# Kernel optimization log

Measured on AMD Instinct MI355X. Metric: run time of the kernel, lower is better.

## Reference

```python
import jax, jax.numpy as jnp
import numpy as np
from jax.scipy.special import gammaln, digamma


def setup_inputs() -> dict:
    key = jax.random.key(0)
    k1, k2 = jax.random.split(key)
    N, M, D = 512, 512, 256
    # Dirichlet concentration parameters: strictly positive
    v_alpha = jax.random.uniform(k1, (N, D), dtype=jnp.float32)
    t_alpha = jax.random.uniform(k2, (M, D), dtype=jnp.float32)
    return {"v_alpha": v_alpha, "t_alpha": t_alpha}


def _compute_kl(v_alpha, t_alpha):
    # v_alpha, t_alpha broadcast to (..., D); returns (...,) KL(Dir(v)||Dir(t))
    eps = 1e-08
    v = v_alpha + eps
    t = t_alpha + eps
    sum_v = v.sum(axis=-1)
    sum_t = t.sum(axis=-1)
    first = (gammaln(t).sum(axis=-1) + gammaln(sum_v)
             - gammaln(sum_t) - gammaln(v).sum(axis=-1))
    second = ((v - t) * (digamma(v) - digamma(sum_v)[..., None])).sum(axis=-1)
    return first + second


def reference(v_alpha, t_alpha):
    # Pairwise JS divergence between all (t_row, v_row) pairs.
    # Original: v.repeat(M,1) / t.repeat_interleave(N) then view(M, N)
    # -> equivalent to broadcasting t over axis 0, v over axis 1.
    v = v_alpha[None, :, :]   # (1, N, D)
    t = t_alpha[:, None, :]   # (M, 1, D)
    m = 0.5 * (v + t)         # (M, N, D)
    jsd = 0.5 * _compute_kl(v, m) + 0.5 * _compute_kl(t, m)  # (M, N)
    return 1.0 - jsd
```

## Files before the change

### kernel.cpp

```cpp
#include <hip/hip_runtime.h>

#define D 256
#define NV 512
#define NT 512
#define KCAT 1536
#define EPS 1e-8f
#define HALF_EPS 5e-9f
#define LN2 0.69314718055994531f

#define C0 0.28468287047291920f
#define C1 0.70315664064524320f
#define C2 0.24517887805011740f
#define C3 (-0.03936734194028790f)
#define C4 0.00932941036738560f
#define C5 (-0.00261463332905590f)
#define C6 0.00080356830356760f
#define C0E 0.28460998445f
#define C1E 0.69577526404f
#define C2E 0.24751123064f

#define LSTRIDE 68

typedef float f32x4 __attribute__((ext_vector_type(4)));
typedef short s16x8 __attribute__((ext_vector_type(8)));
typedef unsigned short u16;

__device__ __forceinline__ float rcpf(float x) { return __builtin_amdgcn_rcpf(x); }

__device__ __forceinline__ u16 f2bf(float f) {
    unsigned int u = __float_as_uint(f);
    return (u16)((u + 0x7FFFu + ((u >> 16) & 1u)) >> 16);
}
__device__ __forceinline__ float bf2f(u16 b) {
    return __uint_as_float(((unsigned int)b) << 16);
}

__device__ __forceinline__ float stirling_lgamma(float y) {
    float r = rcpf(y), r2 = r * r;
    float ln = LN2 * __log2f(y);
    return (y - 0.5f) * ln - y + 0.91893853320467f
         + r * (0.08333333333f - 0.00277777778f * r2);
}

__device__ __forceinline__ float stirling_digamma(float y) {
    float r = rcpf(y), r2 = r * r;
    return LN2 * __log2f(y) - 0.5f * r - r2 * (0.08333333333f - 0.00833333333f * r2);
}

__global__ __launch_bounds__(256) void row_stats(
    const float* __restrict__ va, const float* __restrict__ ta,
    u16* __restrict__ Acat, u16* __restrict__ Bcat,
    float* __restrict__ rv, float* __restrict__ rt)
{
    int r = blockIdx.x;
    bool isV = (r < NV);
    int rr = isV ? r : r - NV;
    const float* row = (isV ? va : ta) + rr * D;
    float* sc = (isV ? rv : rt) + rr * 4;
    u16* cat = (isV ? Bcat : Acat) + rr * KCAT;

    int d = threadIdx.x;
    float raw = row[d];
    float x = raw + EPS;

    float y = x + 4.0f;
    float ry = rcpf(y), ry2 = ry * ry;
    float psi = LN2 * __log2f(y) - 0.5f * ry - ry2 * (0.08333333333f - 0.00833333333f * ry2);
    psi -= rcpf(x) + rcpf(x + 1.0f) + rcpf(x + 2.0f) + rcpf(x + 3.0f);

    float s = x - 0.5f;
    float q6 = fmaf(C6, s, C5);
    q6 = fmaf(q6, s, C4); q6 = fmaf(q6, s, C3); q6 = fmaf(q6, s, C2); q6 = fmaf(q6, s, C1);
    float g = fmaf(q6, s, C0) - LN2 * __log2f(x * (x + 1.0f));

    float pm = psi - C2E * x;
    u16 xh = f2bf(x);  u16 xl = f2bf(x - bf2f(xh));
    u16 ph = f2bf(pm); u16 pl = f2bf(pm - bf2f(ph));
    if (isV) {
        cat[d] = ph; cat[d+256] = pl; cat[d+512] = ph;
        cat[d+768] = xh; cat[d+1024] = xl; cat[d+1280] = xh;
    } else {
        cat[d] = xh; cat[d+256] = xh; cat[d+512] = xl;
        cat[d+768] = ph; cat[d+1024] = ph; cat[d+1280] = pl;
    }

    float vh = fmaf(0.5f, raw, HALF_EPS);
    float S = raw, G = g, P = x * psi, Q = vh * vh;
    #pragma unroll
    for (int off = 32; off > 0; off >>= 1) {
        S += __shfl_down(S, off, 64);
        G += __shfl_down(G, off, 64);
        P += __shfl_down(P, off, 64);
        Q += __shfl_down(Q, off, 64);
    }
    __shared__ float red[4][4];
    int wid = d >> 6, lane = d & 63;
    if (lane == 0) { red[0][wid] = S; red[1][wid] = G; red[2][wid] = P; red[3][wid] = Q; }
    __syncthreads();
    if (d == 0) {
        float S4 = red[0][0] + red[0][1] + red[0][2] + red[0][3];
        float G4 = red[1][0] + red[1][1] + red[1][2] + red[1][3];
        float P4 = red[2][0] + red[2][1] + red[2][2] + red[2][3];
        float Q4 = red[3][0] + red[3][1] + red[3][2] + red[3][3];
        float Se = S4 + 256.0f * EPS;
        float A = 0.5f * (stirling_lgamma(Se) - G4) + 0.25f * P4;
        *(float4*)sc = make_float4(S4, A, stirling_digamma(Se), Q4);
    }
}

__global__ __launch_bounds__(256, 4) void jsd_pairs(
    const float* __restrict__ va, const float* __restrict__ ta,
    const u16* __restrict__ Acat, const u16* __restrict__ Bcat,
    const float* __restrict__ rv, const float* __restrict__ rt,
    float* __restrict__ out)
{
    __shared__ float vs[16 * LSTRIDE];
    __shared__ float ts[16 * LSTRIDE];
    __shared__ float red[4 * 256];

    const int tid = threadIdx.x;
    const int j0 = blockIdx.x * 16;
    const int i0 = blockIdx.y * 16;
    const int w = tid >> 6, l = tid & 63;

    {
        f32x4 acc = {0.0f, 0.0f, 0.0f, 0.0f};
        const u16* Ap = Acat + (i0 + (l & 15)) * KCAT + w * 384 + ((l >> 4) << 3);
        const u16* Bp = Bcat + (j0 + (l & 15)) * KCAT + w * 384 + ((l >> 4) << 3);
        #pragma unroll
        for (int st = 0; st < 12; ++st) {
            s16x8 a = *(const s16x8*)(Ap + (st << 5));
            s16x8 b = *(const s16x8*)(Bp + (st << 5));
            acc = __builtin_amdgcn_mfma_f32_16x16x32_bf16(a, b, acc, 0, 0, 0);
        }
        int base = w * 256 + ((l >> 4) << 6) + (l & 15);
        red[base]      = acc[0];
        red[base + 16] = acc[1];
        red[base + 32] = acc[2];
        red[base + 48] = acc[3];
    }

    const int tj = tid & 15;
    const int ti = tid >> 4;
    const float* vp = vs + tj * LSTRIDE;
    const float* tp = ts + ti * LSTRIDE;
    const int ldst = ti * LSTRIDE + (tj << 2);

    float accLa = 0.0f, accLb = 0.0f;

    for (int h = 0; h < 4; ++h) {
        if (h) __syncthreads();
        {
            int goff = (h << 6) + (tj << 2);
            float4 a = *(const float4*)(va + (j0 + ti) * D + goff);
            float4 e = *(const float4*)(ta + (i0 + ti) * D + goff);
            a.x = fmaf(0.5f, a.x, HALF_EPS); a.y = fmaf(0.5f, a.y, HALF_EPS);
            a.z = fmaf(0.5f, a.z, HALF_EPS); a.w = fmaf(0.5f, a.w, HALF_EPS);
            e.x = fmaf(0.5f, e.x, HALF_EPS); e.y = fmaf(0.5f, e.y, HALF_EPS);
            e.z = fmaf(0.5f, e.z, HALF_EPS); e.w = fmaf(0.5f, e.w, HALF_EPS);
            *(float4*)(vs + ldst) = a;
            *(float4*)(ts + ldst) = e;
        }
        __syncthreads();

        #pragma unroll
        for (int c = 0; c < 16; ++c) {
            float4 v4 = *(const float4*)(vp + (c << 2));
            float4 t4 = *(const float4*)(tp + (c << 2));
            float m0 = v4.x + t4.x, m1 = v4.y + t4.y;
            float m2 = v4.z + t4.z, m3 = v4.w + t4.w;
            float w0 = fmaf(m0, m0, m0), w1 = fmaf(m1, m1, m1);
            float w2 = fmaf(m2, m2, m2), w3 = fmaf(m3, m3, m3);
            float lg = __log2f((w0 * w1) * (w2 * w3));
            if (c & 1) accLb += lg; else accLa += lg;
        }
    }

    const int idx = ti * 16 + tj;
    float W = red[idx] + red[256 + idx] + red[512 + idx] + red[768 + idx];

    const int j = j0 + tj, i = i0 + ti;
    float4 RJ = *(const float4*)(rv + j * 4);
    float4 RI = *(const float4*)(rt + i * 4);
    float Sv = RJ.x, Av = RJ.y, dgSv = RJ.z, Qv = RJ.w;
    float St = RI.x, At = RI.y, dgSt = RI.z, Qt = RI.w;

    float M1 = fmaf(0.5f, Sv + St, 256.0f * EPS);
    float S1 = M1 - 128.0f;
    float quad = Qv + Qt - M1 + 64.0f;
    float sumlg = fmaf(C1E, S1, 256.0f * C0E) + C2E * quad - LN2 * (accLa + accLb);

    float jsd = sumlg - stirling_lgamma(M1) + Av + At
              - 0.25f * W
              + 0.25f * (Sv - St) * (dgSt - dgSv);

    out[i * 512 + j] = 1.0f - jsd;
}

extern "C" void kernel_launch(void* const* d_in, const int* in_sizes, int n_in,
                              void* d_out, int out_size, void* d_ws, size_t ws_size,
                              hipStream_t stream) {
    const float* va = (const float*)d_in[0];
    const float* ta = (const float*)d_in[1];
    float* ws  = (float*)d_ws;
    float* rv  = ws;
    float* rt  = ws + NV * 4;
    u16*   Acat = (u16*)((char*)d_ws + 16384);
    u16*   Bcat = (u16*)((char*)d_ws + 16384 + NV * KCAT * 2);
    float* out = (float*)d_out;

    row_stats<<<NV + NT, 256, 0, stream>>>(va, ta, Acat, Bcat, rv, rt);
    jsd_pairs<<<dim3(32, 32), 256, 0, stream>>>(va, ta, Acat, Bcat, rv, rt, out);
}
```

Baseline: 76.44 us.

## Stage D in two 128-wide halves with register prefetch of second half

Replaces the four 64-column LDS staging rounds with two 128-column rounds, halving the block barriers. The second half's global loads are issued into registers before the first half's compute, so they overlap it. The log-accumulation uses four independent accumulators to shorten the dependency chain. LDS use and register pressure grow, which could lower occupancy under launch_bounds(256,4).

Measured after the change: 80.08 us. +4.8%, slower.

```diff
diff --git a/kernel.cpp b/kernel.cpp
--- a/kernel.cpp
+++ b/kernel.cpp
@@ -19,7 +19,7 @@
 #define C1E 0.69577526404f
 #define C2E 0.24751123064f
 
-#define LSTRIDE 68
+#define LSTRIDE 132
 
 typedef float f32x4 __attribute__((ext_vector_type(4)));
 typedef short s16x8 __attribute__((ext_vector_type(8)));
@@ -140,40 +140,67 @@
         red[base + 48] = acc[3];
     }
 
+    int srow[2], scol[2], sdst[2];
+    #pragma unroll
+    for (int k = 0; k < 2; ++k) {
+        int q = tid + (k << 8);
+        srow[k] = q >> 5;
+        scol[k] = (q & 31) << 2;
+        sdst[k] = srow[k] * LSTRIDE + scol[k];
+    }
+
+    #define HALVE4(P) { P.x = fmaf(0.5f,P.x,HALF_EPS); P.y = fmaf(0.5f,P.y,HALF_EPS); \
+                        P.z = fmaf(0.5f,P.z,HALF_EPS); P.w = fmaf(0.5f,P.w,HALF_EPS); }
+
+    #pragma unroll
+    for (int k = 0; k < 2; ++k) {
+        float4 a = *(const float4*)(va + (j0 + srow[k]) * D + scol[k]);
+        float4 e = *(const float4*)(ta + (i0 + srow[k]) * D + scol[k]);
+        HALVE4(a); HALVE4(e);
+        *(float4*)(vs + sdst[k]) = a;
+        *(float4*)(ts + sdst[k]) = e;
+    }
+    float4 pv[2], pt[2];
+    #pragma unroll
+    for (int k = 0; k < 2; ++k) {
+        pv[k] = *(const float4*)(va + (j0 + srow[k]) * D + 128 + scol[k]);
+        pt[k] = *(const float4*)(ta + (i0 + srow[k]) * D + 128 + scol[k]);
+    }
+    __syncthreads();
+
     const int tj = tid & 15;
     const int ti = tid >> 4;
     const float* vp = vs + tj * LSTRIDE;
     const float* tp = ts + ti * LSTRIDE;
-    const int ldst = ti * LSTRIDE + (tj << 2);
-
-    float accLa = 0.0f, accLb = 0.0f;
-
-    for (int h = 0; h < 4; ++h) {
-        if (h) __syncthreads();
-        {
-            int goff = (h << 6) + (tj << 2);
-            float4 a = *(const float4*)(va + (j0 + ti) * D + goff);
-            float4 e = *(const float4*)(ta + (i0 + ti) * D + goff);
-            a.x = fmaf(0.5f, a.x, HALF_EPS); a.y = fmaf(0.5f, a.y, HALF_EPS);
-            a.z = fmaf(0.5f, a.z, HALF_EPS); a.w = fmaf(0.5f, a.w, HALF_EPS);
-            e.x = fmaf(0.5f, e.x, HALF_EPS); e.y = fmaf(0.5f, e.y, HALF_EPS);
-            e.z = fmaf(0.5f, e.z, HALF_EPS); e.w = fmaf(0.5f, e.w, HALF_EPS);
-            *(float4*)(vs + ldst) = a;
-            *(float4*)(ts + ldst) = e;
-        }
-        __syncthreads();
-
-        #pragma unroll
-        for (int c = 0; c < 16; ++c) {
-            float4 v4 = *(const float4*)(vp + (c << 2));
-            float4 t4 = *(const float4*)(tp + (c << 2));
-            float m0 = v4.x + t4.x, m1 = v4.y + t4.y;
-            float m2 = v4.z + t4.z, m3 = v4.w + t4.w;
-            float w0 = fmaf(m0, m0, m0), w1 = fmaf(m1, m1, m1);
-            float w2 = fmaf(m2, m2, m2), w3 = fmaf(m3, m3, m3);
-            float lg = __log2f((w0 * w1) * (w2 * w3));
-            if (c & 1) accLb += lg; else accLa += lg;
-        }
+
+    float acc0 = 0.0f, acc1 = 0.0f, acc2 = 0.0f, acc3 = 0.0f;
+
+    #define CITER(c, ACC) {                                                   \
+        float4 v4 = *(const float4*)(vp + ((c) << 2));                        \
+        float4 t4 = *(const float4*)(tp + ((c) << 2));                        \
+        float m0 = v4.x + t4.x, m1 = v4.y + t4.y;                             \
+        float m2 = v4.z + t4.z, m3 = v4.w + t4.w;                             \
+        float w0 = fmaf(m0, m0, m0), w1 = fmaf(m1, m1, m1);                   \
+        float w2 = fmaf(m2, m2, m2), w3 = fmaf(m3, m3, m3);                   \
+        ACC += __log2f((w0 * w1) * (w2 * w3)); }
+
+    #pragma unroll
+    for (int c = 0; c < 32; c += 4) {
+        CITER(c + 0, acc0) CITER(c + 1, acc1) CITER(c + 2, acc2) CITER(c + 3, acc3)
+    }
+    __syncthreads();
+
+    #pragma unroll
+    for (int k = 0; k < 2; ++k) {
+        HALVE4(pv[k]); HALVE4(pt[k]);
+        *(float4*)(vs + sdst[k]) = pv[k];
+        *(float4*)(ts + sdst[k]) = pt[k];
+    }
+    __syncthreads();
+
+    #pragma unroll
+    for (int c = 0; c < 32; c += 4) {
+        CITER(c + 0, acc0) CITER(c + 1, acc1) CITER(c + 2, acc2) CITER(c + 3, acc3)
     }
 
     const int idx = ti * 16 + tj;
@@ -188,7 +215,8 @@
     float M1 = fmaf(0.5f, Sv + St, 256.0f * EPS);
     float S1 = M1 - 128.0f;
     float quad = Qv + Qt - M1 + 64.0f;
-    float sumlg = fmaf(C1E, S1, 256.0f * C0E) + C2E * quad - LN2 * (accLa + accLb);
+    float sumlg = fmaf(C1E, S1, 256.0f * C0E) + C2E * quad
+                - LN2 * ((acc0 + acc1) + (acc2 + acc3));
 
     float jsd = sumlg - stirling_lgamma(M1) + Av + At
               - 0.25f * W
```
